# Kernel tuning notes

Hardware: AMD Instinct MI355X
Metric: run time of the kernel (lower is better)

## Reference

```python
import jax, jax.numpy as jnp
import numpy as np

B, S, D, H, DM = 2, 2048, 1024, 16, 4
HD = D // H  # head_dim = 64
EPS = 1e-5


def setup_inputs() -> dict:
    key = jax.random.key(0)
    ks = jax.random.split(key, 8)
    s = 0.02
    return {
        "x": jax.random.normal(ks[0], (B, S, D), jnp.float32),
        "wq": jax.random.normal(ks[1], (D, D), jnp.float32) * s,
        "wk": jax.random.normal(ks[2], (D, D), jnp.float32) * s,
        "wv": jax.random.normal(ks[3], (D, D), jnp.float32) * s,
        "wo": jax.random.normal(ks[4], (D, D), jnp.float32) * s,
        "bo": jnp.zeros((D,), jnp.float32),
        "ln1_scale": jnp.ones((D,), jnp.float32),
        "ln1_shift": jnp.zeros((D,), jnp.float32),
        "ln2_scale": jnp.ones((D,), jnp.float32),
        "ln2_shift": jnp.zeros((D,), jnp.float32),
        "w1": jax.random.normal(ks[5], (DM * D, D), jnp.float32) * s,
        "b1": jnp.zeros((DM * D,), jnp.float32),
        "w2": jax.random.normal(ks[6], (D, DM * D), jnp.float32) * s,
        "b2": jnp.zeros((D,), jnp.float32),
    }


def _layernorm(x, scale, shift):
    mean = jnp.mean(x, axis=-1, keepdims=True)
    var = jnp.var(x, axis=-1, keepdims=True)  # unbiased=False
    return scale * (x - mean) * jax.lax.rsqrt(var + EPS) + shift


def _attn(x, wq, wk, wv, wo, bo):
    b, n, d = x.shape
    # torch Linear: y = x @ W.T
    q = (x @ wq.T).reshape(b, n, H, HD).transpose(0, 2, 1, 3)  # [b,h,n,hd]
    k = (x @ wk.T).reshape(b, n, H, HD).transpose(0, 2, 1, 3)
    v = (x @ wv.T).reshape(b, n, H, HD).transpose(0, 2, 1, 3)
    scores = jnp.einsum("bhqd,bhkd->bhqk", q, k)
    causal = jnp.tril(jnp.ones((n, n), bool))
    scores = jnp.where(causal, scores, -jnp.inf)
    w = jax.nn.softmax(scores / np.sqrt(HD).astype(np.float32), axis=-1)
    ctx = jnp.einsum("bhqk,bhkd->bhqd", w, v)
    ctx = ctx.transpose(0, 2, 1, 3).reshape(b, n, d)
    return ctx @ wo.T + bo


def reference(x, wq, wk, wv, wo, bo, ln1_scale, ln1_shift, ln2_scale, ln2_shift, w1, b1, w2, b2):
    h = x + _attn(_layernorm(x, ln1_scale, ln1_shift), wq, wk, wv, wo, bo)
    y = _layernorm(h, ln2_scale, ln2_shift)
    y = jax.nn.relu(y @ w1.T + b1) @ w2.T + b2
    return h + y
```

## Files before the change

### kernel.cpp

```cpp
#include <hip/hip_runtime.h>
#include <hip/hip_bf16.h>

#define DEV __device__ __forceinline__

typedef __attribute__((ext_vector_type(8))) short bf8;
typedef __attribute__((ext_vector_type(4))) float f4;
typedef __attribute__((ext_vector_type(16))) float f16x;

DEV unsigned short f2bf(float f) {
  union { __hip_bfloat16 h; unsigned short u; } c;
  c.h = __float2bfloat16(f);
  return c.u;
}
DEV unsigned int pk2(float a, float b) {
  union { __hip_bfloat162 h; unsigned int u; } c;
  c.h = __hip_bfloat162(__float2bfloat16(a), __float2bfloat16(b));
  return c.u;
}

DEV int2 swz_tile(int ob, int nxt, int nyt) {
  const int nb = nxt * nyt;
  const int cpx = nb >> 3;
  const int W = (ob & 7) * cpx + (ob >> 3);
  const int scw = 4 * nyt;
  const int sc = W / scw, rem = W - sc * scw;
  return make_int2(rem >> 2, sc * 4 + (rem & 3));
}

template<bool BIAS, bool RELU, bool OUTBF>
__global__ __launch_bounds__(512, 2) void gemm_bt256(
    const unsigned short* __restrict__ A, const unsigned short* __restrict__ B,
    const float* __restrict__ bias, void* __restrict__ Cout,
    int M, int N, int K, int ldc, int nyt)
{
  __shared__ unsigned short Sl[2][2][256 * 64];
  const int t = threadIdx.x;
  const int w = t >> 6, l = t & 63;
  const int wr = w >> 2, wc = w & 3;
  int2 tt = swz_tile((int)blockIdx.x, N >> 8, nyt);
  const int m0 = tt.x * 256, n0 = tt.y * 256;

  const int srow = w * 32 + (l >> 3);
  const int scol = 8 * ((l & 7) ^ (l >> 3));
  const unsigned short* Ab = A + (size_t)(m0 + srow) * K + scol;
  const unsigned short* Bb = B + (size_t)(n0 + srow) * K + scol;
  const int sdst = w * 2048 + l * 8;

  auto STAGE = [&](int slot, int kt) {
#pragma unroll
    for (int i = 0; i < 4; ++i) {
      __builtin_amdgcn_global_load_lds(
          (const __attribute__((address_space(1))) void*)(Ab + (size_t)i * 8 * K + kt * 64),
          (__attribute__((address_space(3))) void*)(&Sl[slot][0][sdst + i * 512]), 16, 0, 0);
      __builtin_amdgcn_global_load_lds(
          (const __attribute__((address_space(1))) void*)(Bb + (size_t)i * 8 * K + kt * 64),
          (__attribute__((address_space(3))) void*)(&Sl[slot][1][sdst + i * 512]), 16, 0, 0);
    }
  };

  const f4 fz = {0.f, 0.f, 0.f, 0.f};
  f4 acc[8][4];
#pragma unroll
  for (int i = 0; i < 8; ++i)
#pragma unroll
    for (int j = 0; j < 4; ++j) acc[i][j] = fz;

  const int NT = K >> 6;
  STAGE(0, 0);
  __syncthreads();

  for (int T = 0; T < NT; ++T) {
    if (T + 1 < NT) STAGE((T + 1) & 1, T + 1);
    const int sl = T & 1;
#pragma unroll
    for (int ks = 0; ks < 2; ++ks) {
      const int cb = (ks * 64 + ((l >> 4) * 16)) ^ ((l & 7) << 4);
      bf8 af[8], bg[4];
#pragma unroll
      for (int m = 0; m < 8; ++m)
        af[m] = *(const bf8*)((const char*)&Sl[sl][0][(wr * 128 + m * 16 + (l & 15)) * 64] + cb);
#pragma unroll
      for (int n = 0; n < 4; ++n)
        bg[n] = *(const bf8*)((const char*)&Sl[sl][1][(wc * 64 + n * 16 + (l & 15)) * 64] + cb);
      __builtin_amdgcn_s_setprio(1);
#pragma unroll
      for (int m = 0; m < 8; ++m)
#pragma unroll
        for (int n = 0; n < 4; ++n)
          acc[m][n] = __builtin_amdgcn_mfma_f32_16x16x32_bf16(af[m], bg[n], acc[m][n], 0, 0, 0);
      __builtin_amdgcn_s_setprio(0);
    }
    __syncthreads();
  }

#pragma unroll
  for (int n = 0; n < 4; ++n) {
    const int col = n0 + wc * 64 + n * 16 + (l & 15);
    float bv = 0.f;
    if (BIAS) bv = bias[col];
#pragma unroll
    for (int m = 0; m < 8; ++m) {
#pragma unroll
      for (int r = 0; r < 4; ++r) {
        const int row = m0 + wr * 128 + m * 16 + ((l >> 4) * 4) + r;
        float v = acc[m][n][r] + bv;
        if (RELU) v = fmaxf(v, 0.f);
        if (OUTBF) ((unsigned short*)Cout)[(size_t)row * ldc + col] = f2bf(v);
        else       ((float*)Cout)[(size_t)row * ldc + col] = v;
      }
    }
  }
}

template<bool BIAS, bool RELU, bool RESID, bool OUTBF, bool WRVT>
__global__ __launch_bounds__(256) void gemm_bt64(
    const unsigned short* __restrict__ A, const unsigned short* __restrict__ B,
    const float* __restrict__ bias, const float* __restrict__ resid,
    void* __restrict__ Cout, int M, int N, int K, int ldc,
    unsigned short* __restrict__ vtout)
{
  __shared__ unsigned short Al[2][64 * 32];
  __shared__ unsigned short Bl[2][128 * 32];
  const int t = threadIdx.x;
  const int w = t >> 6, l = t & 63;
  const int wr = w >> 1, wc = w & 1;
  int2 tt = swz_tile((int)blockIdx.x, N >> 7, M >> 6);
  const int m0 = tt.x * 64, n0 = tt.y * 128;

  const int srow = w * 16 + (l >> 2);
  const int scsw = ((l & 3) * 8) ^ (((srow >> 1) & 3) << 3);
  const unsigned short* Ab = A + (size_t)(m0 + srow) * K + scsw;
  const unsigned short* Bb = B + (size_t)(n0 + srow) * K + scsw;
  const int sdst = w * 512 + l * 8;

  auto STAGE = [&](int slot, int k0) {
    __builtin_amdgcn_global_load_lds(
        (const __attribute__((address_space(1))) void*)(Ab + k0),
        (__attribute__((address_space(3))) void*)(&Al[slot][sdst]), 16, 0, 0);
#pragma unroll
    for (int i = 0; i < 2; ++i) {
      __builtin_amdgcn_global_load_lds(
          (const __attribute__((address_space(1))) void*)(Bb + (size_t)i * 64 * K + k0),
          (__attribute__((address_space(3))) void*)(&Bl[slot][sdst + i * 2048]), 16, 0, 0);
    }
  };

  const f4 fz = {0.f, 0.f, 0.f, 0.f};
  f4 acc[2][4];
#pragma unroll
  for (int i = 0; i < 2; ++i)
#pragma unroll
    for (int j = 0; j < 4; ++j) acc[i][j] = fz;

  const int NT = K >> 5;
  STAGE(0, 0);
  __syncthreads();

  for (int T = 0; T < NT; ++T) {
    if (T + 1 < NT) STAGE((T + 1) & 1, (T + 1) * 32);
    const int sl = T & 1;
    const int rdcol = ((l >> 4) * 8) ^ ((((l & 15) >> 1) & 3) << 3);
    bf8 af[2], bg[4];
#pragma unroll
    for (int am = 0; am < 2; ++am)
      af[am] = *(const bf8*)&Al[sl][(wr * 32 + am * 16 + (l & 15)) * 32 + rdcol];
#pragma unroll
    for (int bn = 0; bn < 4; ++bn)
      bg[bn] = *(const bf8*)&Bl[sl][(wc * 64 + bn * 16 + (l & 15)) * 32 + rdcol];
    __builtin_amdgcn_s_setprio(1);
#pragma unroll
    for (int am = 0; am < 2; ++am)
#pragma unroll
      for (int bn = 0; bn < 4; ++bn)
        acc[am][bn] = __builtin_amdgcn_mfma_f32_16x16x32_bf16(af[am], bg[bn], acc[am][bn], 0, 0, 0);
    __builtin_amdgcn_s_setprio(0);
    __syncthreads();
  }

#pragma unroll
  for (int bn = 0; bn < 4; ++bn) {
    const int col = n0 + wc * 64 + bn * 16 + (l & 15);
    float bv = 0.f;
    if (BIAS) bv = bias[col];
    const bool isv = WRVT && (col >= 2048);
    const int hh = (col - 2048) >> 6, dd = (col - 2048) & 63;
#pragma unroll
    for (int am = 0; am < 2; ++am) {
#pragma unroll
      for (int r = 0; r < 4; ++r) {
        const int row = m0 + wr * 32 + am * 16 + ((l >> 4) * 4) + r;
        float v = acc[am][bn][r] + bv;
        if (RELU) v = fmaxf(v, 0.f);
        if (RESID) v += resid[(size_t)row * ldc + col];
        if (WRVT && isv) {
          const int bb = row >> 11, ss = row & 2047;
          vtout[((size_t)(bb * 16 + hh) * 64 + dd) * 2048 + ss] = f2bf(v);
        } else if (OUTBF) {
          ((unsigned short*)Cout)[(size_t)row * ldc + col] = f2bf(v);
        } else {
          ((float*)Cout)[(size_t)row * ldc + col] = v;
        }
      }
    }
  }
}

__global__ __launch_bounds__(256, 4) void attn_kernel(
    const unsigned short* __restrict__ qk, const unsigned short* __restrict__ vt,
    unsigned short* __restrict__ ctx)
{
  __shared__ unsigned short SM[2][2][64 * 64];

  const int t = threadIdx.x;
  const int w = t >> 6, l = t & 63;
  const int p = w >> 1;
  const int hi = l >> 5, q = l & 31;
  const int bid = blockIdx.x;
  const int xcd = bid & 7, i = bid >> 3;
  const int g = i >> 5, c = i & 31;
  const int s = (g & 1) ? c : 31 - c;
  const int bh = xcd * 4 + g;
  const int b = bh >> 4, h = bh & 15;
  const int tile = 2 * s + (w & 1);
  const int q0w = tile * 32;
  const int h0 = (s + 2) >> 1;

  const unsigned short* qbase = qk + ((size_t)b * 2048) * 2048 + h * 64;
  const unsigned short* kbase = qbase + 1024;
  const unsigned short* vbase = vt + (size_t)bh * 64 * 2048;
  unsigned short* Kl = &SM[p][0][0];
  unsigned short* Vl = &SM[p][1][0];
  const int tp = t & 127;

  bf8 qf[4];
#pragma unroll
  for (int ksl = 0; ksl < 4; ++ksl)
    qf[ksl] = *(const bf8*)(qbase + (size_t)(q0w + q) * 2048 + ksl * 16 + hi * 8);

  f16x oacc[2];
#pragma unroll
  for (int dn = 0; dn < 2; ++dn)
#pragma unroll
    for (int i2 = 0; i2 < 16; ++i2) oacc[dn][i2] = 0.f;
  float m_ = -1e30f, l_ = 0.f;

  for (int it = 0; it < h0; ++it) {
    const int gi = p ? h0 + it : it;
    const bool act = gi <= s;
    __syncthreads();
    if (act) {
#pragma unroll
      for (int ss = 0; ss < 4; ++ss) {
        const int row = ss * 16 + (tp >> 3);
        const int cb = (tp & 7) * 16;
        const int sb = cb ^ ((row & 7) << 4);
        __builtin_amdgcn_global_load_lds(
            (const __attribute__((address_space(1))) void*)
                (kbase + (size_t)(gi * 64 + row) * 2048 + (sb >> 1)),
            (__attribute__((address_space(3))) void*)(&Kl[row * 64 + (cb >> 1)]),
            16, 0, 0);
        __builtin_amdgcn_global_load_lds(
            (const __attribute__((address_space(1))) void*)
                (vbase + (size_t)row * 2048 + gi * 64 + (sb >> 1)),
            (__attribute__((address_space(3))) void*)(&Vl[row * 64 + (cb >> 1)]),
            16, 0, 0);
      }
    }
    __syncthreads();
    if (act) {
      const int kb0 = gi * 64;

      f16x s0, s1;
#pragma unroll
      for (int i2 = 0; i2 < 16; ++i2) { s0[i2] = 0.f; s1[i2] = 0.f; }
      __builtin_amdgcn_s_setprio(1);
#pragma unroll
      for (int ksl = 0; ksl < 4; ++ksl) {
        const int cbq = (ksl * 16 + hi * 8) * 2;
        const int r0 = q, r1 = 32 + q;
        bf8 k0 = *(const bf8*)((const char*)&Kl[r0 * 64] + (cbq ^ ((r0 & 7) << 4)));
        bf8 k1 = *(const bf8*)((const char*)&Kl[r1 * 64] + (cbq ^ ((r1 & 7) << 4)));
        s0 = __builtin_amdgcn_mfma_f32_32x32x16_bf16(k0, qf[ksl], s0, 0, 0, 0);
        s1 = __builtin_amdgcn_mfma_f32_32x32x16_bf16(k1, qf[ksl], s1, 0, 0, 0);
      }
      __builtin_amdgcn_s_setprio(0);

      float pv[32];
      if (gi == s) {
#pragma unroll
        for (int i2 = 0; i2 < 16; ++i2) {
          const int key = kb0 + (i2 & 3) + 8 * (i2 >> 2) + 4 * hi;
          pv[i2]      = (key <= q0w + q)      ? s0[i2] : -1e30f;
          pv[16 + i2] = (key + 32 <= q0w + q) ? s1[i2] : -1e30f;
        }
      } else {
#pragma unroll
        for (int i2 = 0; i2 < 16; ++i2) { pv[i2] = s0[i2]; pv[16 + i2] = s1[i2]; }
      }

      float tm[16];
#pragma unroll
      for (int i2 = 0; i2 < 16; ++i2) tm[i2] = fmaxf(pv[i2], pv[16 + i2]);
#pragma unroll
      for (int st = 8; st >= 1; st >>= 1)
#pragma unroll
        for (int i2 = 0; i2 < 8; ++i2)
          if (i2 < st) tm[i2] = fmaxf(tm[i2], tm[i2 + st]);
      const float pmax = fmaxf(tm[0], __shfl_xor(tm[0], 32));
      if (__any(pmax > m_ + 11.54f)) {
        const float mn = fmaxf(m_, pmax);
        const float alpha = __builtin_amdgcn_exp2f(m_ - mn);
        m_ = mn;
        l_ *= alpha;
#pragma unroll
        for (int dn = 0; dn < 2; ++dn)
#pragma unroll
          for (int i2 = 0; i2 < 16; ++i2) oacc[dn][i2] *= alpha;
      }
#pragma unroll
      for (int i2 = 0; i2 < 32; ++i2) pv[i2] = __builtin_amdgcn_exp2f(pv[i2] - m_);
      float ts[16];
#pragma unroll
      for (int i2 = 0; i2 < 16; ++i2) ts[i2] = pv[i2] + pv[16 + i2];
#pragma unroll
      for (int st = 8; st >= 1; st >>= 1)
#pragma unroll
        for (int i2 = 0; i2 < 8; ++i2)
          if (i2 < st) ts[i2] += ts[i2 + st];
      l_ += ts[0] + __shfl_xor(ts[0], 32);

#pragma unroll
      for (int sg = 0; sg < 2; ++sg) {
        const float* pp = pv + sg * 16;
        unsigned int wds[8];
#pragma unroll
        for (int m = 0; m < 4; ++m) {
          wds[m * 2]     = pk2(pp[4 * m], pp[4 * m + 1]);
          wds[m * 2 + 1] = pk2(pp[4 * m + 2], pp[4 * m + 3]);
        }
#pragma unroll
        for (int kq = 0; kq < 2; ++kq) {
          unsigned int x0 = __shfl_xor((int)(hi ? wds[4 * kq]     : wds[4 * kq + 2]), 32);
          unsigned int x1 = __shfl_xor((int)(hi ? wds[4 * kq + 1] : wds[4 * kq + 3]), 32);
          union { unsigned int u[4]; bf8 v; } pu;
          pu.u[0] = hi ? x0 : wds[4 * kq];
          pu.u[1] = hi ? x1 : wds[4 * kq + 1];
          pu.u[2] = hi ? wds[4 * kq + 2] : x0;
          pu.u[3] = hi ? wds[4 * kq + 3] : x1;
          const bf8 pf = pu.v;
          __builtin_amdgcn_s_setprio(1);
#pragma unroll
          for (int dn = 0; dn < 2; ++dn) {
            const int row = dn * 32 + q;
            const int cb = ((sg * 32 + kq * 16 + hi * 8) * 2) ^ ((row & 7) << 4);
            bf8 vf = *(const bf8*)((const char*)&Vl[row * 64] + cb);
            oacc[dn] = __builtin_amdgcn_mfma_f32_32x32x16_bf16(vf, pf, oacc[dn], 0, 0, 0);
          }
          __builtin_amdgcn_s_setprio(0);
        }
      }
    }
  }

  __syncthreads();
  float* mb = (float*)&SM[0][0][0];
  if (p == 1) {
    float* base = mb + (w & 1) * 2176;
    base[l] = m_;
    base[64 + l] = l_;
#pragma unroll
    for (int dn = 0; dn < 2; ++dn)
#pragma unroll
      for (int i2 = 0; i2 < 16; ++i2)
        base[128 + (dn * 16 + i2) * 64 + l] = oacc[dn][i2];
  }
  __syncthreads();
  if (p == 0) {
    float* base = mb + (w & 1) * 2176;
    const float m2 = base[l], l2 = base[64 + l];
    const float mm = fmaxf(m_, m2);
    const float a0 = __builtin_amdgcn_exp2f(m_ - mm);
    const float a2 = __builtin_amdgcn_exp2f(m2 - mm);
    const float inv = 1.0f / (a0 * l_ + a2 * l2);
    unsigned short* crow = ctx + ((size_t)(b * 2048 + q0w + q)) * 1024 + h * 64;
#pragma unroll
    for (int dn = 0; dn < 2; ++dn)
#pragma unroll
      for (int m = 0; m < 4; ++m) {
        float o0 = a0 * oacc[dn][4 * m]     + a2 * base[128 + (dn * 16 + 4 * m) * 64 + l];
        float o1 = a0 * oacc[dn][4 * m + 1] + a2 * base[128 + (dn * 16 + 4 * m + 1) * 64 + l];
        float o2 = a0 * oacc[dn][4 * m + 2] + a2 * base[128 + (dn * 16 + 4 * m + 2) * 64 + l];
        float o3 = a0 * oacc[dn][4 * m + 3] + a2 * base[128 + (dn * 16 + 4 * m + 3) * 64 + l];
        const int d0 = dn * 32 + 8 * m + 4 * hi;
        *(unsigned int*)(crow + d0)     = pk2(o0 * inv, o1 * inv);
        *(unsigned int*)(crow + d0 + 2) = pk2(o2 * inv, o3 * inv);
      }
  }
}

__global__ __launch_bounds__(256) void ln_kernel(
    const float* __restrict__ x, const float* __restrict__ sc,
    const float* __restrict__ sh, unsigned short* __restrict__ out)
{
  const int row = blockIdx.x, t = threadIdx.x;
  float4 v = ((const float4*)x)[(size_t)row * 256 + t];
  float s = v.x + v.y + v.z + v.w;
  float q = v.x * v.x + v.y * v.y + v.z * v.z + v.w * v.w;
#pragma unroll
  for (int off = 1; off < 64; off <<= 1) {
    s += __shfl_xor(s, off);
    q += __shfl_xor(q, off);
  }
  __shared__ float red[8];
  const int w = t >> 6, l = t & 63;
  if (l == 0) { red[w] = s; red[4 + w] = q; }
  __syncthreads();
  s = red[0] + red[1] + red[2] + red[3];
  q = red[4] + red[5] + red[6] + red[7];
  const float mean = s * (1.0f / 1024.0f);
  const float var = q * (1.0f / 1024.0f) - mean * mean;
  const float rstd = rsqrtf(var + 1e-5f);
  float4 scv = ((const float4*)sc)[t];
  float4 shv = ((const float4*)sh)[t];
  uint2 p;
  p.x = pk2(scv.x * (v.x - mean) * rstd + shv.x, scv.y * (v.y - mean) * rstd + shv.y);
  p.y = pk2(scv.z * (v.z - mean) * rstd + shv.z, scv.w * (v.w - mean) * rstd + shv.w);
  ((uint2*)out)[(size_t)row * 256 + t] = p;
}

__global__ __launch_bounds__(256) void cvt_weights(
    const float* __restrict__ wq, const float* __restrict__ wk,
    const float* __restrict__ wv, const float* __restrict__ wo,
    const float* __restrict__ w1, const float* __restrict__ w2,
    unsigned short* __restrict__ dst)
{
  const int M1 = 1 << 20;
  const int n4 = (12 * M1) / 4;
  const int stride = gridDim.x * 256;
  for (int i4 = blockIdx.x * 256 + threadIdx.x; i4 < n4; i4 += stride) {
    const size_t i = (size_t)i4 * 4;
    const int mi = (int)(i >> 20);
    const float* src;
    size_t off;
    float sc = 1.0f;
    if (mi < 4) {
      src = mi == 0 ? wq : mi == 1 ? wk : mi == 2 ? wv : wo;
      off = i & (size_t)(M1 - 1);
      if (mi == 0) sc = 0.125f * 1.44269504088896f;
    } else if (mi < 8) {
      src = w1; off = i - (size_t)4 * M1;
    } else {
      src = w2; off = i - (size_t)8 * M1;
    }
    float4 v = *(const float4*)(src + off);
    uint2 pq;
    pq.x = pk2(v.x * sc, v.y * sc);
    pq.y = pk2(v.z * sc, v.w * sc);
    ((uint2*)dst)[i4] = pq;
  }
}

extern "C" void kernel_launch(void* const* d_in, const int* in_sizes, int n_in,
                              void* d_out, int out_size, void* d_ws, size_t ws_size,
                              hipStream_t stream)
{
  const float* x    = (const float*)d_in[0];
  const float* wq   = (const float*)d_in[1];
  const float* wk   = (const float*)d_in[2];
  const float* wv   = (const float*)d_in[3];
  const float* wo   = (const float*)d_in[4];
  const float* bo   = (const float*)d_in[5];
  const float* ln1s = (const float*)d_in[6];
  const float* ln1b = (const float*)d_in[7];
  const float* ln2s = (const float*)d_in[8];
  const float* ln2b = (const float*)d_in[9];
  const float* w1   = (const float*)d_in[10];
  const float* b1   = (const float*)d_in[11];
  const float* w2   = (const float*)d_in[12];
  const float* b2   = (const float*)d_in[13];
  float* out = (float*)d_out;

  const int M = 4096;

  unsigned short* ws   = (unsigned short*)d_ws;
  unsigned short* lnb  = ws;
  unsigned short* qkvw = lnb  + (size_t)4096 * 1024;
  unsigned short* wob  = qkvw + (size_t)3072 * 1024;
  unsigned short* w1b  = wob  + (size_t)1024 * 1024;
  unsigned short* w2b  = w1b  + (size_t)4096 * 1024;
  unsigned short* qkb  = w2b  + (size_t)4096 * 1024;
  unsigned short* vtb  = qkb  + (size_t)4096 * 2048;
  unsigned short* ctxb = vtb  + (size_t)32 * 64 * 2048;
  float* hf = (float*)(ctxb + (size_t)4096 * 1024);

  cvt_weights<<<2048, 256, 0, stream>>>(wq, wk, wv, wo, w1, w2, qkvw);

  ln_kernel<<<M, 256, 0, stream>>>(x, ln1s, ln1b, lnb);
  gemm_bt64<false, false, false, true, true><<<1536, 256, 0, stream>>>(
      lnb, qkvw, nullptr, nullptr, qkb, M, 3072, 1024, 2048, vtb);
  attn_kernel<<<1024, 256, 0, stream>>>(qkb, vtb, ctxb);
  gemm_bt64<true, false, true, false, false><<<512, 256, 0, stream>>>(
      ctxb, wob, bo, x, hf, M, 1024, 1024, 1024, nullptr);
  ln_kernel<<<M, 256, 0, stream>>>(hf, ln2s, ln2b, lnb);
  gemm_bt256<true, true, true><<<256, 512, 0, stream>>>(
      lnb, w1b, b1, qkb, M, 4096, 1024, 4096, 16);
  gemm_bt64<true, false, true, false, false><<<512, 256, 0, stream>>>(
      qkb, w2b, b2, hf, out, M, 1024, 4096, 1024, nullptr);
}
```

Baseline: 237.8 us.

## Use triple-buffered LDS pipelines with partial vmcnt waits in GEMM kernels

Both GEMM kernels move from double-buffered LDS staging with two __syncthreads per K-step to a three-slot ring. Loads run two tiles ahead, and each step issues a single barrier after a partial s_waitcnt vmcnt. The 256x256 kernel also cuts its K-tile from 64 to 32 and uses a new row-swizzled LDS layout, which keeps shared memory about the same. The aim is to hide more global-load latency and remove one barrier per iteration, at the cost of more loop iterations and hand-tuned waitcnt counts that must match the number of loads in flight.

```diff
diff --git a/kernel.cpp b/kernel.cpp
--- a/kernel.cpp
+++ b/kernel.cpp
@@ -6,6 +6,11 @@
 typedef __attribute__((ext_vector_type(8))) short bf8;
 typedef __attribute__((ext_vector_type(4))) float f4;
 typedef __attribute__((ext_vector_type(16))) float f16x;
+
+#define GLOAD_LDS(gp, lp) \
+  __builtin_amdgcn_global_load_lds( \
+      (const __attribute__((address_space(1))) void*)(gp), \
+      (__attribute__((address_space(3))) void*)(lp), 16, 0, 0)
 
 DEV unsigned short f2bf(float f) {
   union { __hip_bfloat16 h; unsigned short u; } c;
@@ -33,28 +38,25 @@
     const float* __restrict__ bias, void* __restrict__ Cout,
     int M, int N, int K, int ldc, int nyt)
 {
-  __shared__ unsigned short Sl[2][2][256 * 64];
+  __shared__ unsigned short Al[3][256 * 32];
+  __shared__ unsigned short Bl[3][256 * 32];
   const int t = threadIdx.x;
   const int w = t >> 6, l = t & 63;
   const int wr = w >> 2, wc = w & 3;
   int2 tt = swz_tile((int)blockIdx.x, N >> 8, nyt);
   const int m0 = tt.x * 256, n0 = tt.y * 256;
 
-  const int srow = w * 32 + (l >> 3);
-  const int scol = 8 * ((l & 7) ^ (l >> 3));
-  const unsigned short* Ab = A + (size_t)(m0 + srow) * K + scol;
-  const unsigned short* Bb = B + (size_t)(n0 + srow) * K + scol;
-  const int sdst = w * 2048 + l * 8;
-
-  auto STAGE = [&](int slot, int kt) {
-#pragma unroll
-    for (int i = 0; i < 4; ++i) {
-      __builtin_amdgcn_global_load_lds(
-          (const __attribute__((address_space(1))) void*)(Ab + (size_t)i * 8 * K + kt * 64),
-          (__attribute__((address_space(3))) void*)(&Sl[slot][0][sdst + i * 512]), 16, 0, 0);
-      __builtin_amdgcn_global_load_lds(
-          (const __attribute__((address_space(1))) void*)(Bb + (size_t)i * 8 * K + kt * 64),
-          (__attribute__((address_space(3))) void*)(&Sl[slot][1][sdst + i * 512]), 16, 0, 0);
+  const int sr0 = t >> 2;
+  const int sc0 = ((t & 3) * 8) ^ (((sr0 >> 1) & 3) << 3);
+  const unsigned short* Ab = A + (size_t)(m0 + sr0) * K + sc0;
+  const unsigned short* Bb = B + (size_t)(n0 + sr0) * K + sc0;
+  const int sdst = sr0 * 32 + (t & 3) * 8;
+
+  auto STAGE = [&](int slot, int k0) {
+#pragma unroll
+    for (int i = 0; i < 2; ++i) {
+      GLOAD_LDS(Ab + (size_t)i * 128 * K + k0, &Al[slot][sdst + i * 128 * 32]);
+      GLOAD_LDS(Bb + (size_t)i * 128 * K + k0, &Bl[slot][sdst + i * 128 * 32]);
     }
   };
 
@@ -65,32 +67,34 @@
 #pragma unroll
     for (int j = 0; j < 4; ++j) acc[i][j] = fz;
 
-  const int NT = K >> 6;
+  const int NT = K >> 5;
   STAGE(0, 0);
-  __syncthreads();
+  STAGE(1, 32);
 
   for (int T = 0; T < NT; ++T) {
-    if (T + 1 < NT) STAGE((T + 1) & 1, T + 1);
-    const int sl = T & 1;
-#pragma unroll
-    for (int ks = 0; ks < 2; ++ks) {
-      const int cb = (ks * 64 + ((l >> 4) * 16)) ^ ((l & 7) << 4);
-      bf8 af[8], bg[4];
-#pragma unroll
-      for (int m = 0; m < 8; ++m)
-        af[m] = *(const bf8*)((const char*)&Sl[sl][0][(wr * 128 + m * 16 + (l & 15)) * 64] + cb);
+    if (T + 1 < NT) asm volatile("s_waitcnt vmcnt(4)" ::: "memory");
+    else            asm volatile("s_waitcnt vmcnt(0)" ::: "memory");
+    __builtin_amdgcn_sched_barrier(0);
+    __builtin_amdgcn_s_barrier();
+    __builtin_amdgcn_sched_barrier(0);
+    if (T + 2 < NT) STAGE((T + 2) % 3, (T + 2) * 32);
+
+    const int sl = T % 3;
+    const int rdcol = ((l >> 4) * 8) ^ ((((l & 15) >> 1) & 3) << 3);
+    bf8 af[8], bg[4];
+#pragma unroll
+    for (int m = 0; m < 8; ++m)
+      af[m] = *(const bf8*)&Al[sl][(wr * 128 + m * 16 + (l & 15)) * 32 + rdcol];
+#pragma unroll
+    for (int n = 0; n < 4; ++n)
+      bg[n] = *(const bf8*)&Bl[sl][(wc * 64 + n * 16 + (l & 15)) * 32 + rdcol];
+    __builtin_amdgcn_s_setprio(1);
+#pragma unroll
+    for (int m = 0; m < 8; ++m)
 #pragma unroll
       for (int n = 0; n < 4; ++n)
-        bg[n] = *(const bf8*)((const char*)&Sl[sl][1][(wc * 64 + n * 16 + (l & 15)) * 64] + cb);
-      __builtin_amdgcn_s_setprio(1);
-#pragma unroll
-      for (int m = 0; m < 8; ++m)
-#pragma unroll
-        for (int n = 0; n < 4; ++n)
-          acc[m][n] = __builtin_amdgcn_mfma_f32_16x16x32_bf16(af[m], bg[n], acc[m][n], 0, 0, 0);
-      __builtin_amdgcn_s_setprio(0);
-    }
-    __syncthreads();
+        acc[m][n] = __builtin_amdgcn_mfma_f32_16x16x32_bf16(af[m], bg[n], acc[m][n], 0, 0, 0);
+    __builtin_amdgcn_s_setprio(0);
   }
 
 #pragma unroll
@@ -119,8 +123,8 @@
     void* __restrict__ Cout, int M, int N, int K, int ldc,
     unsigned short* __restrict__ vtout)
 {
-  __shared__ unsigned short Al[2][64 * 32];
-  __shared__ unsigned short Bl[2][128 * 32];
+  __shared__ unsigned short Al[3][64 * 32];
+  __shared__ unsigned short Bl[3][128 * 32];
   const int t = threadIdx.x;
   const int w = t >> 6, l = t & 63;
   const int wr = w >> 1, wc = w & 1;
@@ -134,15 +138,10 @@
   const int sdst = w * 512 + l * 8;
 
   auto STAGE = [&](int slot, int k0) {
-    __builtin_amdgcn_global_load_lds(
-        (const __attribute__((address_space(1))) void*)(Ab + k0),
-        (__attribute__((address_space(3))) void*)(&Al[slot][sdst]), 16, 0, 0);
-#pragma unroll
-    for (int i = 0; i < 2; ++i) {
-      __builtin_amdgcn_global_load_lds(
-          (const __attribute__((address_space(1))) void*)(Bb + (size_t)i * 64 * K + k0),
-          (__attribute__((address_space(3))) void*)(&Bl[slot][sdst + i * 2048]), 16, 0, 0);
-    }
+    GLOAD_LDS(Ab + k0, &Al[slot][sdst]);
+#pragma unroll
+    for (int i = 0; i < 2; ++i)
+      GLOAD_LDS(Bb + (size_t)i * 64 * K + k0, &Bl[slot][sdst + i * 2048]);
   };
 
   const f4 fz = {0.f, 0.f, 0.f, 0.f};
@@ -154,11 +153,17 @@
 
   const int NT = K >> 5;
   STAGE(0, 0);
-  __syncthreads();
+  STAGE(1, 32);
 
   for (int T = 0; T < NT; ++T) {
-    if (T + 1 < NT) STAGE((T + 1) & 1, (T + 1) * 32);
-    const int sl = T & 1;
+    if (T + 1 < NT) asm volatile("s_waitcnt vmcnt(3)" ::: "memory");
+    else            asm volatile("s_waitcnt vmcnt(0)" ::: "memory");
+    __builtin_amdgcn_sched_barrier(0);
+    __builtin_amdgcn_s_barrier();
+    __builtin_amdgcn_sched_barrier(0);
+    if (T + 2 < NT) STAGE((T + 2) % 3, (T + 2) * 32);
+
+    const int sl = T % 3;
     const int rdcol = ((l >> 4) * 8) ^ ((((l & 15) >> 1) & 3) << 3);
     bf8 af[2], bg[4];
 #pragma unroll
@@ -174,7 +179,6 @@
       for (int bn = 0; bn < 4; ++bn)
         acc[am][bn] = __builtin_amdgcn_mfma_f32_16x16x32_bf16(af[am], bg[bn], acc[am][bn], 0, 0, 0);
     __builtin_amdgcn_s_setprio(0);
-    __syncthreads();
   }
 
 #pragma unroll
@@ -254,16 +258,10 @@
         const int row = ss * 16 + (tp >> 3);
         const int cb = (tp & 7) * 16;
         const int sb = cb ^ ((row & 7) << 4);
-        __builtin_amdgcn_global_load_lds(
-            (const __attribute__((address_space(1))) void*)
-                (kbase + (size_t)(gi * 64 + row) * 2048 + (sb >> 1)),
-            (__attribute__((address_space(3))) void*)(&Kl[row * 64 + (cb >> 1)]),
-            16, 0, 0);
-        __builtin_amdgcn_global_load_lds(
-            (const __attribute__((address_space(1))) void*)
-                (vbase + (size_t)row * 2048 + gi * 64 + (sb >> 1)),
-            (__attribute__((address_space(3))) void*)(&Vl[row * 64 + (cb >> 1)]),
-            16, 0, 0);
+        GLOAD_LDS(kbase + (size_t)(gi * 64 + row) * 2048 + (sb >> 1),
+                  &Kl[row * 64 + (cb >> 1)]);
+        GLOAD_LDS(vbase + (size_t)row * 2048 + gi * 64 + (sb >> 1),
+                  &Vl[row * 64 + (cb >> 1)]);
       }
     }
     __syncthreads();
```

New measurement: 272.2 us. +14.5%, slower.
